# Performance work log

Measured on AMD Instinct MI355X. Metric: run time of the kernel, lower is better.

## Reference

```python
import jax, jax.numpy as jnp
import numpy as np

B, S, E, H = 2, 2048, 1024, 16
DH = E // H


def setup_inputs() -> dict:
    key = jax.random.key(0)
    ks = jax.random.split(key, 9)
    inp = {
        "query": jax.random.normal(ks[0], (B, S, E), dtype=jnp.float32),
        "key": jax.random.normal(ks[1], (B, S, E), dtype=jnp.float32),
        "value": jax.random.normal(ks[2], (B, S, E), dtype=jnp.float32),
        # causal mask: True means "masked out" (masked_fill semantics)
        "mask": jnp.broadcast_to(
            jnp.triu(jnp.ones((S, S), dtype=bool), k=1)[None, None], (B, 1, S, S)
        ),
        # learned parameters (nn.Linear weight is [out, in]; y = x @ W.T + b)
        "Wq": jax.random.normal(ks[3], (E, E), dtype=jnp.float32) / np.sqrt(E),
        "Wk": jax.random.normal(ks[4], (E, E), dtype=jnp.float32) / np.sqrt(E),
        "Wv": jax.random.normal(ks[5], (E, E), dtype=jnp.float32) / np.sqrt(E),
        "Wo": jax.random.normal(ks[6], (E, E), dtype=jnp.float32) / np.sqrt(E),
        "bo": jax.random.normal(ks[7], (E,), dtype=jnp.float32) * 0.01,
    }
    return inp


def reference(query, key, value, mask, Wq, Wk, Wv, Wo, bo):
    # projections (no bias for q/k/v)
    Q = query @ Wq.T  # [B,S,E]
    K = key @ Wk.T
    V = value @ Wv.T
    # split heads: [B,S,E] -> [B,H,S,Dh]
    Q = Q.reshape(B, S, H, DH).transpose(0, 2, 1, 3)
    K = K.reshape(B, S, H, DH).transpose(0, 2, 1, 3)
    V = V.reshape(B, S, H, DH).transpose(0, 2, 1, 3)
    scale = 1.0 / np.sqrt(DH).astype(np.float32)
    scores = jnp.einsum("bhqd,bhkd->bhqk", Q, K) * scale  # [B,H,S,S]
    scores = jnp.where(mask, -jnp.inf, scores)
    attn = jax.nn.softmax(scores, axis=-1)
    # dropout(p=0.2) is identity in eval mode
    out = jnp.einsum("bhqk,bhkd->bhqd", attn, V)  # [B,H,S,Dh]
    out = out.transpose(0, 2, 1, 3).reshape(B, S, E)
    return out @ Wo.T + bo
```

## Files before the change

### kernel.cpp

```cpp
#include <hip/hip_runtime.h>
#include <hip/hip_bf16.h>
#include <stdint.h>

#define Bb 2
#define Ss 2048
#define Ee 1024
#define Hh 16
#define Dh 64

typedef __bf16 bf16_t;
typedef __attribute__((ext_vector_type(8))) __bf16 bf16x8;
typedef __attribute__((ext_vector_type(4))) __bf16 bf16x4;
typedef __attribute__((ext_vector_type(4))) float f32x4;

#define QSCALE_LOG2E 0.18033688011112042f

__device__ inline void gload_lds16(const void* g, void* l) {
  __builtin_amdgcn_global_load_lds((__attribute__((address_space(1))) void*)g,
                                   (__attribute__((address_space(3))) void*)l,
                                   16, 0, 0);
}

struct Cvt7 {
  const float* s[7];
  bf16_t* d[7];
  int n8[7];
};

__global__ __launch_bounds__(256) void cvt_f32_bf16(Cvt7 c) {
  int gid = blockIdx.x * 256 + threadIdx.x;
#pragma unroll
  for (int j = 0; j < 7; ++j) {
    if (gid < c.n8[j]) {
      const float* s = c.s[j] + (size_t)gid * 8;
      const f32x4 lo = *(const f32x4*)s;
      const f32x4 hi = *(const f32x4*)(s + 4);
      bf16x8 v;
      v[0] = (bf16_t)lo[0]; v[1] = (bf16_t)lo[1];
      v[2] = (bf16_t)lo[2]; v[3] = (bf16_t)lo[3];
      v[4] = (bf16_t)hi[0]; v[5] = (bf16_t)hi[1];
      v[6] = (bf16_t)hi[2]; v[7] = (bf16_t)hi[3];
      *(bf16x8*)(c.d[j] + (size_t)gid * 8) = v;
      return;
    }
    gid -= c.n8[j];
  }
}

template <int ROWS>
__device__ __forceinline__ void stage_bf16(const bf16_t* __restrict__ src,
                                           int ldk, int k0, bf16_t* lds,
                                           int wave, int lane) {
  const int srow = lane >> 3, sslot = lane & 7;
#pragma unroll
  for (int r = 0; r < ROWS / 32; ++r) {
    const int chunk = wave + r * 4;
    const int row = chunk * 8 + srow;
    const int k16 = sslot ^ (row & 7);
    gload_lds16(src + (size_t)row * ldk + k0 + k16 * 8, lds + chunk * 512);
  }
}

__device__ __forceinline__ void mfma_tile_128(const bf16_t* As,
                                              const bf16_t* Bs, int wr, int wc,
                                              int lr, int lg, f32x4 acc[4][4]) {
  const char* a_base = (const char*)As;
  const char* b_base = (const char*)Bs;
#pragma unroll
  for (int kk = 0; kk < 2; ++kk) {
    bf16x8 af[4], bfr[4];
#pragma unroll
    for (int x = 0; x < 4; ++x) {
      const int arow = wr * 64 + x * 16 + lr;
      af[x] = *(const bf16x8*)(a_base + ((arow * 128 + kk * 64 + lg * 16) ^
                                         ((arow & 7) << 4)));
      const int brow = wc * 64 + x * 16 + lr;
      bfr[x] = *(const bf16x8*)(b_base + ((brow * 128 + kk * 64 + lg * 16) ^
                                          ((brow & 7) << 4)));
    }
#pragma unroll
    for (int mi = 0; mi < 4; ++mi)
#pragma unroll
      for (int ni = 0; ni < 4; ++ni)
        acc[mi][ni] = __builtin_amdgcn_mfma_f32_16x16x32_bf16(
            af[mi], bfr[ni], acc[mi][ni], 0, 0, 0);
  }
}

__global__ __launch_bounds__(256) void qkv_proj(
    const bf16_t* __restrict__ Aq, const bf16_t* __restrict__ Ak,
    const bf16_t* __restrict__ Av, const bf16_t* __restrict__ Wq,
    const bf16_t* __restrict__ Wk, const bf16_t* __restrict__ Wv,
    bf16_t* __restrict__ Cq, bf16_t* __restrict__ Ck,
    bf16_t* __restrict__ Cv) {
  __shared__ bf16_t As[128 * 64];
  __shared__ bf16_t Bs[128 * 64];
  const int z = blockIdx.z;
  const bf16_t* A = (z == 0) ? Aq : (z == 1) ? Ak : Av;
  const bf16_t* W = (z == 0) ? Wq : (z == 1) ? Wk : Wv;
  bf16_t* C = (z == 0) ? Cq : (z == 1) ? Ck : Cv;

  const int wg = blockIdx.y * 8 + blockIdx.x;
  const int virt = (wg & 7) * 32 + (wg >> 3);
  const int n0 = (virt & 7) * 128, m0 = (virt >> 3) * 128;

  const int tid = threadIdx.x;
  const int lane = tid & 63, wave = tid >> 6;
  const int wr = wave >> 1, wc = wave & 1;
  const int lr = lane & 15, lg = lane >> 4;

  f32x4 acc[4][4] = {};

  for (int k0 = 0; k0 < Ee; k0 += 64) {
    stage_bf16<128>(A + (size_t)m0 * Ee, Ee, k0, As, wave, lane);
    stage_bf16<128>(W + (size_t)n0 * Ee, Ee, k0, Bs, wave, lane);
    asm volatile("s_waitcnt vmcnt(0)" ::: "memory");
    __syncthreads();
    mfma_tile_128(As, Bs, wr, wc, lr, lg, acc);
    __syncthreads();
  }

#pragma unroll
  for (int mi = 0; mi < 4; ++mi) {
#pragma unroll
    for (int i = 0; i < 4; ++i) {
      const int m = m0 + wr * 64 + mi * 16 + lg * 4 + i;
#pragma unroll
      for (int ni = 0; ni < 4; ++ni) {
        const int n = n0 + wc * 64 + ni * 16 + lr;
        float v = acc[mi][ni][i];
        if (z == 0) v *= QSCALE_LOG2E;
        const int b = m >> 11, s = m & (Ss - 1);
        const int h = n >> 6, d = n & 63;
        if (z != 2)
          C[(((size_t)(b * Hh + h)) * Ss + s) * Dh + d] = (bf16_t)v;
        else
          C[(((size_t)(b * Hh + h)) * Dh + d) * Ss + s] = (bf16_t)v;
      }
    }
  }
}

__global__ __launch_bounds__(256) void out_gemm(const bf16_t* __restrict__ A,
                                                const bf16_t* __restrict__ W,
                                                const float* __restrict__ bias,
                                                float* __restrict__ C) {
  __shared__ bf16_t As[128 * 64];
  __shared__ bf16_t Bs[64 * 64];
  const int wg = blockIdx.y * 16 + blockIdx.x;
  const int virt = (wg & 7) * 64 + (wg >> 3);
  const int n0 = (virt & 15) * 64, m0 = (virt >> 4) * 128;

  const int tid = threadIdx.x;
  const int lane = tid & 63, wave = tid >> 6;
  const int lr = lane & 15, lg = lane >> 4;

  f32x4 acc[2][4] = {};

  for (int k0 = 0; k0 < Ee; k0 += 64) {
    stage_bf16<128>(A + (size_t)m0 * Ee, Ee, k0, As, wave, lane);
    stage_bf16<64>(W + (size_t)n0 * Ee, Ee, k0, Bs, wave, lane);
    asm volatile("s_waitcnt vmcnt(0)" ::: "memory");
    __syncthreads();

    const char* a_base = (const char*)As;
    const char* b_base = (const char*)Bs;
#pragma unroll
    for (int kk = 0; kk < 2; ++kk) {
      bf16x8 af[2], bfr[4];
#pragma unroll
      for (int x = 0; x < 2; ++x) {
        const int arow = wave * 32 + x * 16 + lr;
        af[x] = *(const bf16x8*)(a_base + ((arow * 128 + kk * 64 + lg * 16) ^
                                           ((arow & 7) << 4)));
      }
#pragma unroll
      for (int ni = 0; ni < 4; ++ni) {
        const int brow = ni * 16 + lr;
        bfr[ni] = *(const bf16x8*)(b_base + ((brow * 128 + kk * 64 + lg * 16) ^
                                             ((brow & 7) << 4)));
      }
#pragma unroll
      for (int mi = 0; mi < 2; ++mi)
#pragma unroll
        for (int ni = 0; ni < 4; ++ni)
          acc[mi][ni] = __builtin_amdgcn_mfma_f32_16x16x32_bf16(
              af[mi], bfr[ni], acc[mi][ni], 0, 0, 0);
    }
    __syncthreads();
  }

#pragma unroll
  for (int mi = 0; mi < 2; ++mi) {
#pragma unroll
    for (int i = 0; i < 4; ++i) {
      const int m = m0 + wave * 32 + mi * 16 + lg * 4 + i;
#pragma unroll
      for (int ni = 0; ni < 4; ++ni) {
        const int n = n0 + ni * 16 + lr;
        C[(size_t)m * Ee + n] = acc[mi][ni][i] + bias[n];
      }
    }
  }
}


__device__ __forceinline__ void attn_stage(const bf16_t* Kh, const bf16_t* Vh,
                                           int kv0, int wave, int lane,
                                           bf16_t* KsBuf, bf16_t* VsBuf) {
#pragma unroll
  for (int r = 0; r < 4; ++r) {
    const int c = wave + r * 4;
    const int krow = c * 8 + (lane >> 3);
    const int ks = (lane & 7) ^ (krow & 7);
    gload_lds16(Kh + (size_t)(kv0 + krow) * Dh + ks * 8, KsBuf + c * 512);
    const int vrow = c * 4 + (lane >> 4);
    const int vs = (lane & 15) ^ (vrow & 7);
    gload_lds16(Vh + (size_t)vrow * Ss + kv0 + vs * 8, VsBuf + c * 512);
  }
}

template <int NI, bool MASKED>
__device__ __forceinline__ void attn_tile_compute(
    int kv0, int qw, int lane, char* pb, const char* kb, const char* vb,
    const bf16x8 aq[2], float& m_run, float& l_run, f32x4 oacc[4]) {
  const int lr = lane & 15, lg = lane >> 4;

  f32x4 sc[NI];
#pragma unroll
  for (int ni = 0; ni < NI; ++ni) {
    const int krow = ni * 16 + lr;
    const bf16x8 ak0 =
        *(const bf16x8*)(kb + ((krow * 128 + lg * 16) ^ ((krow & 7) << 4)));
    const bf16x8 ak1 = *(const bf16x8*)(kb + ((krow * 128 + 64 + lg * 16) ^
                                              ((krow & 7) << 4)));
    f32x4 z = {0.f, 0.f, 0.f, 0.f};
    z = __builtin_amdgcn_mfma_f32_16x16x32_bf16(ak0, aq[0], z, 0, 0, 0);
    z = __builtin_amdgcn_mfma_f32_16x16x32_bf16(ak1, aq[1], z, 0, 0, 0);
    sc[ni] = z;
  }

  if (MASKED) {
    const int q_rel = qw + lr - kv0;
#pragma unroll
    for (int ni = 0; ni < NI; ++ni)
#pragma unroll
      for (int i = 0; i < 4; ++i)
        if (ni * 16 + lg * 4 + i > q_rel) sc[ni][i] = -1e30f;
  }

  f32x4 vm = sc[0];
#pragma unroll
  for (int ni = 1; ni < NI; ++ni)
#pragma unroll
    for (int i = 0; i < 4; ++i) vm[i] = fmaxf(vm[i], sc[ni][i]);
  float rm = fmaxf(fmaxf(vm[0], vm[1]), fmaxf(vm[2], vm[3]));
  rm = fmaxf(rm, __shfl_xor(rm, 16));
  rm = fmaxf(rm, __shfl_xor(rm, 32));

  const float mo = m_run;
  const float mn = fmaxf(mo, rm);
  const float corr = __builtin_amdgcn_exp2f(mo - mn);
  m_run = mn;

  f32x4 vs = {0.f, 0.f, 0.f, 0.f};
#pragma unroll
  for (int ni = 0; ni < NI; ++ni) {
    bf16x4 w;
#pragma unroll
    for (int i = 0; i < 4; ++i) {
      const float p = __builtin_amdgcn_exp2f(sc[ni][i] - mn);
      vs[i] += p;
      w[i] = (bf16_t)p;
    }
    *(bf16x4*)(pb + ((lr * 256 + ni * 32 + lg * 8) ^ ((lr & 7) << 4))) = w;
  }
  float rs = (vs[0] + vs[1]) + (vs[2] + vs[3]);
  rs += __shfl_xor(rs, 16);
  rs += __shfl_xor(rs, 32);
  l_run = l_run * corr + rs;

#pragma unroll
  for (int i = 0; i < 4; ++i) {
    const float ci = __shfl(corr, (lane & 48) | (lg * 4 + i));
#pragma unroll
    for (int di = 0; di < 4; ++di) oacc[di][i] *= ci;
  }

#pragma unroll
  for (int kk = 0; kk < NI / 2; ++kk) {
    const bf16x8 pa = *(const bf16x8*)(pb + ((lr * 256 + kk * 64 + lg * 16) ^
                                             ((lr & 7) << 4)));
#pragma unroll
    for (int di = 0; di < 4; ++di) {
      const int vrow = di * 16 + lr;
      const bf16x8 bv = *(const bf16x8*)(vb + ((vrow * 256 + kk * 64 +
                                                lg * 16) ^
                                               ((vrow & 7) << 4)));
      oacc[di] =
          __builtin_amdgcn_mfma_f32_16x16x32_bf16(pa, bv, oacc[di], 0, 0, 0);
    }
  }
}

__device__ __forceinline__ void flash_qtile(int qt, const bf16_t* Qh,
                                            const bf16_t* Kh, const bf16_t* Vh,
                                            bf16_t* AO_row, int wave, int lane,
                                            bf16_t* Ks, bf16_t* Vs,
                                            bf16_t* PsW) {
  const int lr = lane & 15, lg = lane >> 4;
  const int qw = qt * 64 + wave * 16;

  bf16x8 aq[2];
#pragma unroll
  for (int kd = 0; kd < 2; ++kd)
    aq[kd] = *(const bf16x8*)(Qh + (size_t)(qw + lr) * Dh + kd * 32 + lg * 8);

  f32x4 oacc[4] = {};
  float m_run = -1e30f, l_run = 0.f;
  char* pb = (char*)PsW;

  const int nt = (qt + 2) >> 1;
  attn_stage(Kh, Vh, 0, wave, lane, Ks, Vs);
  asm volatile("s_waitcnt vmcnt(0)" ::: "memory");
  __syncthreads();

  for (int t = 0; t < nt; ++t) {
    const int cur = t & 1;
    if (t + 1 < nt)
      attn_stage(Kh, Vh, (t + 1) * 128, wave, lane, Ks + (cur ^ 1) * 8192,
                 Vs + (cur ^ 1) * 8192);
    const char* kb = (const char*)(Ks + cur * 8192);
    const char* vb = (const char*)(Vs + cur * 8192);
    if (t < nt - 1)
      attn_tile_compute<8, false>(t * 128, qw, lane, pb, kb, vb, aq, m_run,
                                  l_run, oacc);
    else if ((qt & 1) == 0)
      attn_tile_compute<4, true>(t * 128, qw, lane, pb, kb, vb, aq, m_run,
                                 l_run, oacc);
    else
      attn_tile_compute<8, true>(t * 128, qw, lane, pb, kb, vb, aq, m_run,
                                 l_run, oacc);
    asm volatile("s_waitcnt vmcnt(0)" ::: "memory");
    __syncthreads();
  }

#pragma unroll
  for (int i = 0; i < 4; ++i) {
    const float li = __shfl(l_run, (lane & 48) | (lg * 4 + i));
    const float inv = 1.0f / li;
    const int s = qw + lg * 4 + i;
#pragma unroll
    for (int di = 0; di < 4; ++di) {
      const int d = di * 16 + lr;
      AO_row[(size_t)s * Ee + d] = (bf16_t)(oacc[di][i] * inv);
    }
  }
}

__global__ __launch_bounds__(256, 2) void attn_causal(
    const bf16_t* __restrict__ Qg, const bf16_t* __restrict__ Kg,
    const bf16_t* __restrict__ Vg, bf16_t* __restrict__ AO) {
  const int wg = blockIdx.y * 16 + blockIdx.x;
  const int virt = (wg & 7) * 64 + (wg >> 3);
  const int qx = virt & 15;
  const int bh = virt >> 4;

  const int tid = threadIdx.x;
  const int lane = tid & 63, wave = tid >> 6;

  const bf16_t* Qh = Qg + (size_t)bh * Ss * Dh;
  const bf16_t* Kh = Kg + (size_t)bh * Ss * Dh;
  const bf16_t* Vh = Vg + (size_t)bh * Dh * Ss;
  const int b = bh >> 4, h = bh & 15;
  bf16_t* AO_row = AO + (size_t)b * Ss * Ee + h * 64;

  __shared__ bf16_t Ks[2][128 * 64];
  __shared__ bf16_t Vs[2][64 * 128];
  __shared__ bf16_t Ps[4][16 * 128];

  const int qtA = qx;
  const int qtB = 31 - qx;
  flash_qtile(qtA, Qh, Kh, Vh, AO_row, wave, lane, Ks[0], Vs[0], Ps[wave]);
  flash_qtile(qtB, Qh, Kh, Vh, AO_row, wave, lane, Ks[0], Vs[0], Ps[wave]);
}

extern "C" void kernel_launch(void* const* d_in, const int* in_sizes, int n_in,
                              void* d_out, int out_size, void* d_ws,
                              size_t ws_size, hipStream_t stream) {
  const float* query = (const float*)d_in[0];
  const float* key = (const float*)d_in[1];
  const float* value = (const float*)d_in[2];
  const float* Wq = (const float*)d_in[4];
  const float* Wk = (const float*)d_in[5];
  const float* Wv = (const float*)d_in[6];
  const float* Wo = (const float*)d_in[7];
  const float* bo = (const float*)d_in[8];

  const size_t T = (size_t)Bb * Ss * Ee;
  const size_t WN = (size_t)Ee * Ee;
  bf16_t* qbf = (bf16_t*)d_ws;
  bf16_t* kbf = qbf + T;
  bf16_t* vbf = kbf + T;
  bf16_t* wqb = vbf + T;
  bf16_t* wkb = wqb + WN;
  bf16_t* wvb = wkb + WN;
  bf16_t* wob = wvb + WN;
  bf16_t* qws = wob + WN;
  bf16_t* kws = qws + T;
  bf16_t* vws = kws + T;
  bf16_t* aows = qbf;

  Cvt7 c;
  c.s[0] = query; c.d[0] = qbf; c.n8[0] = (int)(T / 8);
  c.s[1] = key;   c.d[1] = kbf; c.n8[1] = (int)(T / 8);
  c.s[2] = value; c.d[2] = vbf; c.n8[2] = (int)(T / 8);
  c.s[3] = Wq;    c.d[3] = wqb; c.n8[3] = (int)(WN / 8);
  c.s[4] = Wk;    c.d[4] = wkb; c.n8[4] = (int)(WN / 8);
  c.s[5] = Wv;    c.d[5] = wvb; c.n8[5] = (int)(WN / 8);
  c.s[6] = Wo;    c.d[6] = wob; c.n8[6] = (int)(WN / 8);
  const int total8 = (int)((3 * T + 4 * WN) / 8);

  dim3 blk(256);
  cvt_f32_bf16<<<dim3(total8 / 256), blk, 0, stream>>>(c);
  qkv_proj<<<dim3(Ee / 128, (Bb * Ss) / 128, 3), blk, 0, stream>>>(
      qbf, kbf, vbf, wqb, wkb, wvb, qws, kws, vws);
  attn_causal<<<dim3(16, Bb * Hh), blk, 0, stream>>>(qws, kws, vws, aows);
  out_gemm<<<dim3(Ee / 64, (Bb * Ss) / 128), blk, 0, stream>>>(
      aows, wob, bo, (float*)d_out);
}
```

Baseline: 122.3 us.

## Double-buffer LDS tiles in QKV projection and output GEMMs

Both the QKV projection GEMM and the output projection GEMM now use two LDS buffers per operand. The next K-slice is prefetched with global_load_lds while MFMAs run on the current slice, with one wait and barrier per iteration instead of two. The goal is to hide global memory latency behind compute. In exchange, LDS usage doubles (64KB for qkv_proj), which may reduce occupancy.

```diff
diff --git a/kernel.cpp b/kernel.cpp
--- a/kernel.cpp
+++ b/kernel.cpp
@@ -93,8 +93,8 @@
     const bf16_t* __restrict__ Wk, const bf16_t* __restrict__ Wv,
     bf16_t* __restrict__ Cq, bf16_t* __restrict__ Ck,
     bf16_t* __restrict__ Cv) {
-  __shared__ bf16_t As[128 * 64];
-  __shared__ bf16_t Bs[128 * 64];
+  __shared__ bf16_t As[2][128 * 64];
+  __shared__ bf16_t Bs[2][128 * 64];
   const int z = blockIdx.z;
   const bf16_t* A = (z == 0) ? Aq : (z == 1) ? Ak : Av;
   const bf16_t* W = (z == 0) ? Wq : (z == 1) ? Wk : Wv;
@@ -109,15 +109,26 @@
   const int wr = wave >> 1, wc = wave & 1;
   const int lr = lane & 15, lg = lane >> 4;
 
+  const bf16_t* Arow = A + (size_t)m0 * Ee;
+  const bf16_t* Wrow = W + (size_t)n0 * Ee;
+
   f32x4 acc[4][4] = {};
 
-  for (int k0 = 0; k0 < Ee; k0 += 64) {
-    stage_bf16<128>(A + (size_t)m0 * Ee, Ee, k0, As, wave, lane);
-    stage_bf16<128>(W + (size_t)n0 * Ee, Ee, k0, Bs, wave, lane);
+  stage_bf16<128>(Arow, Ee, 0, As[0], wave, lane);
+  stage_bf16<128>(Wrow, Ee, 0, Bs[0], wave, lane);
+  asm volatile("s_waitcnt vmcnt(0)" ::: "memory");
+  __syncthreads();
+
+  int cur = 0;
+  for (int t = 0; t < Ee / 64; ++t) {
+    if (t + 1 < Ee / 64) {
+      stage_bf16<128>(Arow, Ee, (t + 1) * 64, As[cur ^ 1], wave, lane);
+      stage_bf16<128>(Wrow, Ee, (t + 1) * 64, Bs[cur ^ 1], wave, lane);
+    }
+    mfma_tile_128(As[cur], Bs[cur], wr, wc, lr, lg, acc);
     asm volatile("s_waitcnt vmcnt(0)" ::: "memory");
     __syncthreads();
-    mfma_tile_128(As, Bs, wr, wc, lr, lg, acc);
-    __syncthreads();
+    cur ^= 1;
   }
 
 #pragma unroll
@@ -145,8 +156,8 @@
                                                 const bf16_t* __restrict__ W,
                                                 const float* __restrict__ bias,
                                                 float* __restrict__ C) {
-  __shared__ bf16_t As[128 * 64];
-  __shared__ bf16_t Bs[64 * 64];
+  __shared__ bf16_t As[2][128 * 64];
+  __shared__ bf16_t Bs[2][64 * 64];
   const int wg = blockIdx.y * 16 + blockIdx.x;
   const int virt = (wg & 7) * 64 + (wg >> 3);
   const int n0 = (virt & 15) * 64, m0 = (virt >> 4) * 128;
@@ -155,16 +166,25 @@
   const int lane = tid & 63, wave = tid >> 6;
   const int lr = lane & 15, lg = lane >> 4;
 
+  const bf16_t* Arow = A + (size_t)m0 * Ee;
+  const bf16_t* Wrow = W + (size_t)n0 * Ee;
+
   f32x4 acc[2][4] = {};
 
-  for (int k0 = 0; k0 < Ee; k0 += 64) {
-    stage_bf16<128>(A + (size_t)m0 * Ee, Ee, k0, As, wave, lane);
-    stage_bf16<64>(W + (size_t)n0 * Ee, Ee, k0, Bs, wave, lane);
-    asm volatile("s_waitcnt vmcnt(0)" ::: "memory");
-    __syncthreads();
-
-    const char* a_base = (const char*)As;
-    const char* b_base = (const char*)Bs;
+  stage_bf16<128>(Arow, Ee, 0, As[0], wave, lane);
+  stage_bf16<64>(Wrow, Ee, 0, Bs[0], wave, lane);
+  asm volatile("s_waitcnt vmcnt(0)" ::: "memory");
+  __syncthreads();
+
+  int cur = 0;
+  for (int t = 0; t < Ee / 64; ++t) {
+    if (t + 1 < Ee / 64) {
+      stage_bf16<128>(Arow, Ee, (t + 1) * 64, As[cur ^ 1], wave, lane);
+      stage_bf16<64>(Wrow, Ee, (t + 1) * 64, Bs[cur ^ 1], wave, lane);
+    }
+
+    const char* a_base = (const char*)As[cur];
+    const char* b_base = (const char*)Bs[cur];
 #pragma unroll
     for (int kk = 0; kk < 2; ++kk) {
       bf16x8 af[2], bfr[4];
@@ -187,7 +207,9 @@
           acc[mi][ni] = __builtin_amdgcn_mfma_f32_16x16x32_bf16(
               af[mi], bfr[ni], acc[mi][ni], 0, 0, 0);
     }
+    asm volatile("s_waitcnt vmcnt(0)" ::: "memory");
     __syncthreads();
+    cur ^= 1;
   }
 
 #pragma unroll
```

Result: slower. 132.0 us (+7.9%).
